# Optimization experiments

Hardware: AMD Instinct MI355X
Metric: run time of the kernel (lower is better)

Reference implementation:

```python
import jax, jax.numpy as jnp
import numpy as np

B, N, C = 8, 1024, 768
H, D = 12, 64
SCALE = D ** -0.5
EPS = 1e-5

def layernorm(x, g, b):
    mu = jnp.mean(x, axis=-1, keepdims=True)
    var = jnp.var(x, axis=-1, keepdims=True)
    return (x - mu) * jax.lax.rsqrt(var + EPS) * g + b

def setup_inputs() -> dict:
    key = jax.random.key(0)
    ks = jax.random.split(key, 5)
    return {
        "x": jax.random.normal(ks[0], (B, N, C), jnp.float32),
        "qkv_w": jax.random.normal(ks[1], (3 * C, C), jnp.float32) * 0.02,
        "qkv_b": jax.random.normal(ks[2], (3 * C,), jnp.float32) * 0.02,
        "qn_g": jnp.ones((D,), jnp.float32),
        "qn_b": jnp.zeros((D,), jnp.float32),
        "kn_g": jnp.ones((D,), jnp.float32),
        "kn_b": jnp.zeros((D,), jnp.float32),
        "proj_w": jax.random.normal(ks[3], (C, C), jnp.float32) * 0.02,
        "proj_b": jnp.zeros((C,), jnp.float32),
    }

def reference(x, qkv_w, qkv_b, qn_g, qn_b, kn_g, kn_b, proj_w, proj_b):
    # qkv projection: [B,N,3C] -> [3,B,H,N,D]
    qkv = jnp.einsum('bnc,oc->bno', x, qkv_w) + qkv_b
    qkv = qkv.reshape(B, N, 3, H, D).transpose(2, 0, 3, 1, 4)
    q, k, v = qkv[0], qkv[1], qkv[2]
    q = layernorm(q, qn_g, qn_b) * SCALE
    k = layernorm(k, kn_g, kn_b)
    # explicit attention matrix [B,H,N,N] (module stores it)
    attn = jax.nn.softmax(jnp.einsum('bhqd,bhkd->bhqk', q, k), axis=-1)
    out = jnp.einsum('bhqk,bhkd->bhqd', attn, v)
    out = out.transpose(0, 2, 1, 3).reshape(B, N, C)
    out = jnp.einsum('bnc,oc->bno', out, proj_w) + proj_b
    return out
```

## Files before the change

kernel.cpp:

```cpp
#include <hip/hip_runtime.h>
#include <cstdint>

#define Bz 8
#define Nn 1024
#define Cc 768
#define Hh 12
#define Dd 64
#define C3 2304
#define BN 8192

constexpr float EPS = 1e-5f;
constexpr float QSCALE = 0.125f * 1.44269504088896340736f;

typedef __attribute__((ext_vector_type(8))) short bf16x8;
typedef _Float16 f16x8 __attribute__((ext_vector_type(8)));
typedef __attribute__((ext_vector_type(4))) float f32x4;
typedef __attribute__((ext_vector_type(16))) float f32x16;

__device__ __forceinline__ short f2b(float f) {
    union { float f; unsigned u; } x; x.f = f;
    unsigned r = x.u + 0x7FFFu + ((x.u >> 16) & 1u);
    return (short)(r >> 16);
}
__device__ __forceinline__ unsigned cvtpk(float a, float b) {
    unsigned r;
    asm("v_cvt_pk_bf16_f32 %0, %1, %2" : "=v"(r) : "v"(a), "v"(b));
    return r;
}

__device__ __forceinline__ f32x4 MFMAH(f16x8 a, f16x8 b, f32x4 c) {
    return __builtin_amdgcn_mfma_f32_16x16x32_f16(a, b, c, 0, 0, 0);
}
__device__ __forceinline__ f32x16 MFMA32(bf16x8 a, bf16x8 b, f32x16 c) {
    return __builtin_amdgcn_mfma_f32_32x32x16_bf16(a, b, c, 0, 0, 0);
}
__device__ __forceinline__ f16x8 ldf16(const _Float16* p) { return *(const f16x8*)p; }
__device__ __forceinline__ void gld16(const void* g, void* l) {
    __builtin_amdgcn_global_load_lds((const __attribute__((address_space(1))) unsigned int*)g,
                                     (__attribute__((address_space(3))) unsigned int*)(l),
                                     16, 0, 0);
}
__device__ __forceinline__ void waitv8() { asm volatile("s_waitcnt vmcnt(8)" ::: "memory"); }
__device__ __forceinline__ void waitv4() { asm volatile("s_waitcnt vmcnt(4)" ::: "memory"); }
__device__ __forceinline__ void waitv0() { asm volatile("s_waitcnt vmcnt(0)" ::: "memory"); }

__global__ __launch_bounds__(256) void cvt_all(
    const float* __restrict__ x, const float* __restrict__ wq, const float* __restrict__ wp,
    _Float16* __restrict__ xh, _Float16* __restrict__ wqh, _Float16* __restrict__ wph)
{
    const int n1 = BN * Cc / 8, n2 = n1 + C3 * Cc / 8, n3 = n2 + Cc * Cc / 8;
    int i = blockIdx.x * 256 + threadIdx.x;
    const float* s; _Float16* d; int off;
    if (i < n1)      { s = x;  d = xh;  off = i; }
    else if (i < n2) { s = wq; d = wqh; off = i - n1; }
    else if (i < n3) { s = wp; d = wph; off = i - n2; }
    else return;
    float4 a = *(const float4*)(s + (size_t)off * 8);
    float4 b = *(const float4*)(s + (size_t)off * 8 + 4);
    f16x8 o;
    o[0] = (_Float16)a.x; o[1] = (_Float16)a.y; o[2] = (_Float16)a.z; o[3] = (_Float16)a.w;
    o[4] = (_Float16)b.x; o[5] = (_Float16)b.y; o[6] = (_Float16)b.z; o[7] = (_Float16)b.w;
    *(f16x8*)(d + (size_t)off * 8) = o;
}

template<int EPI>
__global__ __launch_bounds__(256, 2) void gemm_f16(
    const _Float16* __restrict__ A,
    const _Float16* __restrict__ W,
    const float* __restrict__ bias,
    float* __restrict__ Out,
    short* __restrict__ qp, short* __restrict__ kp, short* __restrict__ vp,
    const float* __restrict__ qg, const float* __restrict__ qb,
    const float* __restrict__ kg, const float* __restrict__ kb,
    int nx)
{
    __shared__ _Float16 As[4][128 * 32];
    __shared__ _Float16 Bs[4][128 * 32];
    const int tid = threadIdx.x;
    const int lane = tid & 63;
    const int w = tid >> 6;
    const int wr = w >> 1, wc = w & 1;
    const int l15 = lane & 15, l4 = lane >> 4;

    const int chunk = gridDim.x >> 3;
    const int wg = (blockIdx.x & 7) * chunk + (blockIdx.x >> 3);
    const int by = wg / nx;
    int bx = wg % nx;
    if (by & 1) bx = nx - 1 - bx;
    const int m0 = by * 128;
    const int n0 = bx * 128;

    auto stage = [&](int kt, int buf) {
        const int k0 = kt * 32;
#pragma unroll
        for (int j = 0; j < 4; ++j) {
            int i = w * 4 + j;
            int isA = (i < 8);
            int ib = isA ? i : i - 8;
            int row = ib * 16 + (lane >> 2);
            int gslot = (lane & 3) ^ ((row + (row >> 2)) & 3);
            const _Float16* src = (isA ? A + (size_t)(m0 + row) * 768
                                       : W + (size_t)(n0 + row) * 768) + k0 + gslot * 8;
            _Float16* dst = (isA ? &As[buf][0] : &Bs[buf][0]) + ib * 512;
            gld16(src, dst);
        }
    };

    f32x4 acc[4][4];
#pragma unroll
    for (int mi = 0; mi < 4; ++mi)
#pragma unroll
        for (int ni = 0; ni < 4; ++ni) { acc[mi][ni][0]=0.f; acc[mi][ni][1]=0.f; acc[mi][ni][2]=0.f; acc[mi][ni][3]=0.f; }

    auto compute = [&](int buf) {
        f16x8 af[4], bfr[4];
#pragma unroll
        for (int mi = 0; mi < 4; ++mi) {
            int row = wr * 64 + mi * 16 + l15;
            int slot = l4 ^ ((row + (row >> 2)) & 3);
            af[mi] = ldf16(&As[buf][row * 32 + slot * 8]);
        }
#pragma unroll
        for (int ni = 0; ni < 4; ++ni) {
            int row = wc * 64 + ni * 16 + l15;
            int slot = l4 ^ ((row + (row >> 2)) & 3);
            bfr[ni] = ldf16(&Bs[buf][row * 32 + slot * 8]);
        }
#pragma unroll
        for (int mi = 0; mi < 4; ++mi)
#pragma unroll
            for (int ni = 0; ni < 4; ++ni)
                acc[mi][ni] = MFMAH(af[mi], bfr[ni], acc[mi][ni]);
    };

    stage(0, 0); stage(1, 1); stage(2, 2);
    for (int t = 0; t < 22; ++t) {
        waitv8();
        __builtin_amdgcn_s_barrier();
        if (t < 21) stage(t + 3, (t + 3) & 3);
        compute(t & 3);
    }
    waitv4(); __builtin_amdgcn_s_barrier(); compute(22 & 3);
    waitv0(); __builtin_amdgcn_s_barrier(); compute(23 & 3);

    if (EPI == 0) {
#pragma unroll
        for (int mi = 0; mi < 4; ++mi)
#pragma unroll
            for (int r = 0; r < 4; ++r) {
                int row = m0 + wr * 64 + mi * 16 + l4 * 4 + r;
#pragma unroll
                for (int ni = 0; ni < 4; ++ni) {
                    int col = n0 + wc * 64 + ni * 16 + l15;
                    Out[(size_t)row * Cc + col] = acc[mi][ni][r] + bias[col];
                }
            }
    } else {
        const int ncol0 = n0 + wc * 64;
        const int type = ncol0 / Cc;
        const int h = (ncol0 % Cc) >> 6;
        const float* gptr = (type == 0) ? qg : kg;
        const float* bptr = (type == 0) ? qb : kb;
        float biasv[4], gv[4], bv[4];
#pragma unroll
        for (int ni = 0; ni < 4; ++ni) {
            int d = ni * 16 + l15;
            biasv[ni] = bias[ncol0 + d];
            if (type < 2) { gv[ni] = gptr[d]; bv[ni] = bptr[d]; }
        }
        short* plane = (type == 0) ? qp : (type == 1) ? kp : vp;
#pragma unroll
        for (int mi = 0; mi < 4; ++mi)
#pragma unroll
            for (int r = 0; r < 4; ++r) {
                float v[4];
#pragma unroll
                for (int ni = 0; ni < 4; ++ni) v[ni] = acc[mi][ni][r] + biasv[ni];
                int row = m0 + wr * 64 + mi * 16 + l4 * 4 + r;
                size_t base = ((size_t)row * Hh + h) * 64;
                if (type < 2) {
                    float s = v[0] + v[1] + v[2] + v[3];
#pragma unroll
                    for (int off = 1; off < 16; off <<= 1) s += __shfl_xor(s, off);
                    float mu = s * (1.0f / 64.0f);
                    float s2 = 0.f;
#pragma unroll
                    for (int ni = 0; ni < 4; ++ni) { float dv = v[ni] - mu; s2 += dv * dv; }
#pragma unroll
                    for (int off = 1; off < 16; off <<= 1) s2 += __shfl_xor(s2, off);
                    float inv = rsqrtf(s2 * (1.0f / 64.0f) + EPS);
#pragma unroll
                    for (int ni = 0; ni < 4; ++ni) {
                        float rr = (v[ni] - mu) * inv * gv[ni] + bv[ni];
                        if (type == 0) rr *= QSCALE;
                        plane[base + ni * 16 + l15] = f2b(rr);
                    }
                } else {
#pragma unroll
                    for (int ni = 0; ni < 4; ++ni)
                        plane[base + ni * 16 + l15] = f2b(v[ni]);
                }
            }
    }
}

__global__ __launch_bounds__(256, 4) void flash_attn_mfma(
    const short* __restrict__ qp, const short* __restrict__ kp, const short* __restrict__ vp,
    _Float16* __restrict__ att)
{
    __shared__ short kls[2][64 * 64];
    __shared__ short vtl[2][64 * 64];
    const int tid = threadIdx.x;
    const int lane = tid & 63;
    const int w = tid >> 6;
    const int l31 = lane & 31;
    const int hi = lane >> 5;
    const int lr = lane >> 3;
    const int lslot = lane & 7;
    const int bid = (blockIdx.x & 7) * 96 + (blockIdx.x >> 3);
    const int qt = bid & 7;
    const int bh = bid >> 3;
    const int h = bh % Hh;
    const int b = bh / Hh;
    const int q0 = qt * 128;
    const size_t hbase = ((size_t)b * Nn * Hh + h) * 64;
    const int n0v = (tid & 31) * 2, d0v = (tid >> 5) * 8;
    const int khalf = n0v & 31;
    const int t2v = n0v >> 5;
    const int ksig = khalf ^ ((((khalf >> 2) ^ (khalf >> 3)) & 1) * 12);
    const int colv = t2v * 32 + ksig;

    bf16x8 qf[4];
    {
        const short* qsrc = qp + hbase + (size_t)(q0 + w * 32 + l31) * 768 + hi * 8;
#pragma unroll
        for (int ds = 0; ds < 4; ++ds)
            qf[ds] = *(const bf16x8*)(qsrc + ds * 16);
    }

    auto kstage = [&](int kt, int buf) {
#pragma unroll
        for (int i = 0; i < 2; ++i) {
            int row = i * 32 + w * 8 + lr;
            gld16(kp + hbase + (size_t)(kt * 64 + row) * 768 + (lslot ^ lr) * 8,
                  &kls[buf][(i * 32 + w * 8) * 64]);
        }
    };
    auto vcommit = [&](int buf, bf16x8 a0, bf16x8 a1) {
#pragma unroll
        for (int j = 0; j < 8; ++j) {
            int d = d0v + j;
            int fv = (d ^ (d >> 3)) & 7;
            unsigned pku = (unsigned short)a0[j] | ((unsigned)(unsigned short)a1[j] << 16);
            *(unsigned*)&vtl[buf][d * 64 + (((colv >> 3) ^ fv) << 3) + (colv & 7)] = pku;
        }
    };

    kstage(0, 0);
    {
        const short* s0 = vp + hbase + (size_t)n0v * 768 + d0v;
        vcommit(0, *(const bf16x8*)s0, *(const bf16x8*)(s0 + 768));
    }
    __syncthreads();

    f32x16 o0, o1;
#pragma unroll
    for (int i = 0; i < 16; ++i) { o0[i] = 0.f; o1[i] = 0.f; }
    float lrun = 0.f;

    for (int kt = 0; kt < 16; ++kt) {
        const int cur = kt & 1, nxt = cur ^ 1;
        bf16x8 va0, va1;
        if (kt < 15) {
            kstage(kt + 1, nxt);
            const short* s0 = vp + hbase + (size_t)((kt + 1) * 64 + n0v) * 768 + d0v;
            va0 = *(const bf16x8*)s0;
            va1 = *(const bf16x8*)(s0 + 768);
        }
        unsigned pk[2][8];
#pragma unroll
        for (int t2 = 0; t2 < 2; ++t2) {
            f32x16 st;
#pragma unroll
            for (int i = 0; i < 16; ++i) st[i] = 0.f;
            const int row = t2 * 32 + l31;
            __builtin_amdgcn_s_setprio(1);
#pragma unroll
            for (int ds = 0; ds < 4; ++ds) {
                bf16x8 kf = *(const bf16x8*)&kls[cur][row * 64 + (((ds * 2 + hi) ^ (row & 7)) << 3)];
                st = MFMA32(kf, qf[ds], st);
            }
            __builtin_amdgcn_s_setprio(0);
#pragma unroll
            for (int i = 0; i < 16; ++i) st[i] = exp2f(st[i]);
            {
                float s01 = (st[0] + st[1]) + (st[2] + st[3]);
                float s23 = (st[4] + st[5]) + (st[6] + st[7]);
                float s45 = (st[8] + st[9]) + (st[10] + st[11]);
                float s67 = (st[12] + st[13]) + (st[14] + st[15]);
                lrun += (s01 + s23) + (s45 + s67);
            }
#pragma unroll
            for (int i = 0; i < 8; ++i) pk[t2][i] = cvtpk(st[2 * i], st[2 * i + 1]);
        }
        __builtin_amdgcn_s_setprio(1);
#pragma unroll
        for (int t2 = 0; t2 < 2; ++t2)
#pragma unroll
            for (int c = 0; c < 2; ++c) {
                union { bf16x8 v; unsigned u[4]; } a;
                a.u[0] = pk[t2][c * 4 + 0]; a.u[1] = pk[t2][c * 4 + 1];
                a.u[2] = pk[t2][c * 4 + 2]; a.u[3] = pk[t2][c * 4 + 3];
#pragma unroll
                for (int nt = 0; nt < 2; ++nt) {
                    int r = nt * 32 + l31;
                    int fv = (r ^ (r >> 3)) & 7;
                    bf16x8 vf = *(const bf16x8*)&vtl[cur][r * 64 + (((t2 * 4 + c * 2 + hi) ^ fv) << 3)];
                    if (nt == 0) o0 = MFMA32(a.v, vf, o0);
                    else         o1 = MFMA32(a.v, vf, o1);
                }
            }
        __builtin_amdgcn_s_setprio(0);
        if (kt < 15) vcommit(nxt, va0, va1);
        __syncthreads();
    }

    lrun += __shfl_xor(lrun, 32);
    float linv = 1.0f / lrun;
#pragma unroll
    for (int r = 0; r < 16; ++r) {
        int qr = (r & 3) + 8 * (r >> 2) + 4 * hi;
        float invr = __shfl(linv, qr);
        int row = q0 + w * 32 + qr;
        _Float16* dst = att + (size_t)(b * Nn + row) * Cc + h * 64 + l31;
        dst[0]  = (_Float16)(o0[r] * invr);
        dst[32] = (_Float16)(o1[r] * invr);
    }
}

extern "C" void kernel_launch(void* const* d_in, const int* in_sizes, int n_in,
                              void* d_out, int out_size, void* d_ws, size_t ws_size,
                              hipStream_t stream)
{
    const float* x      = (const float*)d_in[0];
    const float* qkv_w  = (const float*)d_in[1];
    const float* qkv_b  = (const float*)d_in[2];
    const float* qn_g   = (const float*)d_in[3];
    const float* qn_b   = (const float*)d_in[4];
    const float* kn_g   = (const float*)d_in[5];
    const float* kn_b   = (const float*)d_in[6];
    const float* proj_w = (const float*)d_in[7];
    const float* proj_b = (const float*)d_in[8];
    float* out = (float*)d_out;

    char* ws = (char*)d_ws;
    short*    qp  = (short*)(ws);
    short*    kp  = (short*)(ws + 12582912);
    short*    vp  = (short*)(ws + 25165824);
    _Float16* att = (_Float16*)(ws + 37748736);
    _Float16* xh  = (_Float16*)(ws + 50331648);
    _Float16* wqh = (_Float16*)(ws + 62914560);
    _Float16* wph = (_Float16*)(ws + 66453504);

    {
        const int n3 = BN * Cc / 8 + C3 * Cc / 8 + Cc * Cc / 8;
        cvt_all<<<(n3 + 255) / 256, 256, 0, stream>>>(x, qkv_w, proj_w, xh, wqh, wph);
    }
    gemm_f16<1><<<(BN / 128) * (C3 / 128), 256, 0, stream>>>(
        xh, wqh, qkv_b, nullptr, qp, kp, vp, qn_g, qn_b, kn_g, kn_b, C3 / 128);
    flash_attn_mfma<<<Bz * Hh * 8, 256, 0, stream>>>(qp, kp, vp, att);
    gemm_f16<0><<<(BN / 128) * (Cc / 128), 256, 0, stream>>>(
        att, wph, proj_b, out, nullptr, nullptr, nullptr, nullptr, nullptr, nullptr, nullptr, Cc / 128);
}
```

Measured before the change: 135.7 us.

## Replace 4-stage LDS pipeline with single-buffer BK=64 GEMM at higher occupancy

Replaces the four-deep BK=32 LDS ring buffer with a single BK=64 buffer and XOR swizzle, which cuts LDS use from 64KB to 32KB. Launch bounds rise from 2 to 4 blocks per CU. Global loads for the next tile are issued only after compute finishes, so intra-block overlap is gone and latency hiding must come from the extra resident blocks. The GEMM also does two barriers per k-tile instead of one.

```diff
diff --git a/kernel.cpp b/kernel.cpp
--- a/kernel.cpp
+++ b/kernel.cpp
@@ -40,9 +40,6 @@
                                      (__attribute__((address_space(3))) unsigned int*)(l),
                                      16, 0, 0);
 }
-__device__ __forceinline__ void waitv8() { asm volatile("s_waitcnt vmcnt(8)" ::: "memory"); }
-__device__ __forceinline__ void waitv4() { asm volatile("s_waitcnt vmcnt(4)" ::: "memory"); }
-__device__ __forceinline__ void waitv0() { asm volatile("s_waitcnt vmcnt(0)" ::: "memory"); }
 
 __global__ __launch_bounds__(256) void cvt_all(
     const float* __restrict__ x, const float* __restrict__ wq, const float* __restrict__ wp,
@@ -64,7 +61,7 @@
 }
 
 template<int EPI>
-__global__ __launch_bounds__(256, 2) void gemm_f16(
+__global__ __launch_bounds__(256, 4) void gemm_f16(
     const _Float16* __restrict__ A,
     const _Float16* __restrict__ W,
     const float* __restrict__ bias,
@@ -74,13 +71,15 @@
     const float* __restrict__ kg, const float* __restrict__ kb,
     int nx)
 {
-    __shared__ _Float16 As[4][128 * 32];
-    __shared__ _Float16 Bs[4][128 * 32];
+    __shared__ _Float16 As[128 * 64];
+    __shared__ _Float16 Bs[128 * 64];
     const int tid = threadIdx.x;
     const int lane = tid & 63;
     const int w = tid >> 6;
     const int wr = w >> 1, wc = w & 1;
     const int l15 = lane & 15, l4 = lane >> 4;
+    const int lr = lane >> 3;
+    const int lslot = lane & 7;
 
     const int chunk = gridDim.x >> 3;
     const int wg = (blockIdx.x & 7) * chunk + (blockIdx.x >> 3);
@@ -90,18 +89,18 @@
     const int m0 = by * 128;
     const int n0 = bx * 128;
 
-    auto stage = [&](int kt, int buf) {
-        const int k0 = kt * 32;
-#pragma unroll
-        for (int j = 0; j < 4; ++j) {
-            int i = w * 4 + j;
-            int isA = (i < 8);
-            int ib = isA ? i : i - 8;
-            int row = ib * 16 + (lane >> 2);
-            int gslot = (lane & 3) ^ ((row + (row >> 2)) & 3);
+    auto stage = [&](int kt) {
+        const int k0 = kt * 64;
+#pragma unroll
+        for (int j = 0; j < 8; ++j) {
+            int i = w * 8 + j;
+            int isA = (i < 16);
+            int ib = isA ? i : i - 16;
+            int row = ib * 8 + lr;
+            int gslot = lslot ^ (row & 7);
             const _Float16* src = (isA ? A + (size_t)(m0 + row) * 768
                                        : W + (size_t)(n0 + row) * 768) + k0 + gslot * 8;
-            _Float16* dst = (isA ? &As[buf][0] : &Bs[buf][0]) + ib * 512;
+            _Float16* dst = (isA ? As : Bs) + ib * 512;
             gld16(src, dst);
         }
     };
@@ -112,36 +111,33 @@
 #pragma unroll
         for (int ni = 0; ni < 4; ++ni) { acc[mi][ni][0]=0.f; acc[mi][ni][1]=0.f; acc[mi][ni][2]=0.f; acc[mi][ni][3]=0.f; }
 
-    auto compute = [&](int buf) {
-        f16x8 af[4], bfr[4];
-#pragma unroll
-        for (int mi = 0; mi < 4; ++mi) {
-            int row = wr * 64 + mi * 16 + l15;
-            int slot = l4 ^ ((row + (row >> 2)) & 3);
-            af[mi] = ldf16(&As[buf][row * 32 + slot * 8]);
-        }
-#pragma unroll
-        for (int ni = 0; ni < 4; ++ni) {
-            int row = wc * 64 + ni * 16 + l15;
-            int slot = l4 ^ ((row + (row >> 2)) & 3);
-            bfr[ni] = ldf16(&Bs[buf][row * 32 + slot * 8]);
-        }
-#pragma unroll
-        for (int mi = 0; mi < 4; ++mi)
-#pragma unroll
-            for (int ni = 0; ni < 4; ++ni)
-                acc[mi][ni] = MFMAH(af[mi], bfr[ni], acc[mi][ni]);
-    };
-
-    stage(0, 0); stage(1, 1); stage(2, 2);
-    for (int t = 0; t < 22; ++t) {
-        waitv8();
-        __builtin_amdgcn_s_barrier();
-        if (t < 21) stage(t + 3, (t + 3) & 3);
-        compute(t & 3);
-    }
-    waitv4(); __builtin_amdgcn_s_barrier(); compute(22 & 3);
-    waitv0(); __builtin_amdgcn_s_barrier(); compute(23 & 3);
+    stage(0);
+    for (int kt = 0; kt < 12; ++kt) {
+        __syncthreads();
+#pragma unroll
+        for (int ks = 0; ks < 2; ++ks) {
+            f16x8 af[4], bfr[4];
+#pragma unroll
+            for (int mi = 0; mi < 4; ++mi) {
+                int row = wr * 64 + mi * 16 + l15;
+                int slot = (ks * 4 + l4) ^ (row & 7);
+                af[mi] = ldf16(&As[row * 64 + slot * 8]);
+            }
+#pragma unroll
+            for (int ni = 0; ni < 4; ++ni) {
+                int row = wc * 64 + ni * 16 + l15;
+                int slot = (ks * 4 + l4) ^ (row & 7);
+                bfr[ni] = ldf16(&Bs[row * 64 + slot * 8]);
+            }
+#pragma unroll
+            for (int mi = 0; mi < 4; ++mi)
+#pragma unroll
+                for (int ni = 0; ni < 4; ++ni)
+                    acc[mi][ni] = MFMAH(af[mi], bfr[ni], acc[mi][ni]);
+        }
+        __syncthreads();
+        if (kt < 11) stage(kt + 1);
+    }
 
     if (EPI == 0) {
 #pragma unroll
```

After: 126.5 us. -6.8%, faster.
